# Performance work log

Measured on AMD Instinct MI355X. Metric: run time of the kernel, lower is better.

Reference implementation:

```python
import jax, jax.numpy as jnp
import numpy as np

EMBED_DIM = 2048
NUM_HEADS = 16
NUM_KV_GROUPS = 4
HEAD_DIM = EMBED_DIM // NUM_HEADS  # 128


def setup_inputs() -> dict:
    key = jax.random.key(0)
    ks = jax.random.split(key, 9)
    B, S, E = 2, 2048, EMBED_DIM
    kv_dim = HEAD_DIM * NUM_KV_GROUPS
    sc = 1.0 / np.sqrt(E)
    return {
        "x": jax.random.normal(ks[0], (B, S, E), dtype=jnp.float32),
        "Wq": jax.random.normal(ks[1], (E, E), dtype=jnp.float32) * sc,
        "bq": jnp.zeros((E,), dtype=jnp.float32),
        "Wk": jax.random.normal(ks[2], (E, kv_dim), dtype=jnp.float32) * sc,
        "bk": jnp.zeros((kv_dim,), dtype=jnp.float32),
        "Wv": jax.random.normal(ks[3], (E, kv_dim), dtype=jnp.float32) * sc,
        "bv": jnp.zeros((kv_dim,), dtype=jnp.float32),
        "Wo": jax.random.normal(ks[4], (E, E), dtype=jnp.float32) * sc,
        "bo": jnp.zeros((E,), dtype=jnp.float32),
    }


def reference(x, Wq, bq, Wk, bk, Wv, bv, Wo, bo):
    B, S, E = x.shape
    H, G, D = NUM_HEADS, NUM_KV_GROUPS, HEAD_DIM
    R = H // G  # heads per kv group
    # projections
    Q = (x @ Wq + bq).reshape(B, S, H, D).transpose(0, 2, 1, 3)   # [B,H,S,D]
    K = (x @ Wk + bk).reshape(B, S, G, D).transpose(0, 2, 1, 3)   # [B,G,S,D]
    V = (x @ Wv + bv).reshape(B, S, G, D).transpose(0, 2, 1, 3)   # [B,G,S,D]
    # GQA: broadcast KV groups over head subgroups instead of repeat_interleave copy
    Qg = Q.reshape(B, G, R, S, D)
    scores = jnp.einsum('bgrsd,bgtd->bgrst', Qg, K) / np.sqrt(D)  # [B,G,R,S,S]
    weights = jax.nn.softmax(scores, axis=-1)
    out = jnp.einsum('bgrst,bgtd->bgrsd', weights, V)             # [B,G,R,S,D]
    out = out.reshape(B, H, S, D).transpose(0, 2, 1, 3).reshape(B, S, E)
    return out @ Wo + bo
```

## Files before the change

kernel.cpp:

```cpp
#include <hip/hip_runtime.h>
#include <hip/hip_bf16.h>


typedef __attribute__((ext_vector_type(8))) short bf16x8;
typedef __attribute__((ext_vector_type(4))) short bf16x4;
typedef __attribute__((ext_vector_type(4))) float f32x4;

#define MFMA_16x16x32(a, b, c) __builtin_amdgcn_mfma_f32_16x16x32_bf16((a), (b), (c), 0, 0, 0)

__device__ __forceinline__ unsigned short f2bf(float x) {
  union { float f; unsigned int u; } c;
  c.f = x;
  unsigned int u = c.u;
  return (unsigned short)((u + 0x7fffu + ((u >> 16) & 1u)) >> 16);
}

__device__ __forceinline__ unsigned short f2bf_hw(float x) {
  __hip_bfloat16 h = __float2bfloat16(x);
  union { __hip_bfloat16 h; unsigned short u; } c;
  c.h = h;
  return c.u;
}

__device__ __forceinline__ void gload_lds16(const void* g, void* l) {
  __builtin_amdgcn_global_load_lds(
      (const __attribute__((address_space(1))) unsigned int*)g,
      (__attribute__((address_space(3))) unsigned int*)l, 16, 0, 0);
}

__global__ void cast_x_kernel(const float* __restrict__ x,
                              unsigned short* __restrict__ out, long n) {
  long i = ((long)blockIdx.x * blockDim.x + threadIdx.x) * 8;
  if (i >= n) return;
  float4 a = *reinterpret_cast<const float4*>(x + i);
  float4 b = *reinterpret_cast<const float4*>(x + i + 4);
  union { unsigned short s[8]; bf16x8 v; } o;
  o.s[0] = f2bf(a.x); o.s[1] = f2bf(a.y); o.s[2] = f2bf(a.z); o.s[3] = f2bf(a.w);
  o.s[4] = f2bf(b.x); o.s[5] = f2bf(b.y); o.s[6] = f2bf(b.z); o.s[7] = f2bf(b.w);
  *reinterpret_cast<bf16x8*>(out + i) = o.v;
}

__global__ void prep_w_kernel(const float* __restrict__ Wq,
                              const float* __restrict__ Wk,
                              const float* __restrict__ Wv,
                              const float* __restrict__ Wo,
                              unsigned short* __restrict__ WqkvT,
                              unsigned short* __restrict__ WoT) {
  __shared__ float t[32][33];
  const int tx = threadIdx.x, ty = threadIdx.y;
  const int ng = blockIdx.x * 32;
  const int k0 = blockIdx.y * 32;
  const float* src;
  int srcN, n0;
  unsigned short* dst;
  if (ng < 2048)      { src = Wq; srcN = 2048; n0 = ng;        dst = WqkvT + (size_t)ng * 2048; }
  else if (ng < 2560) { src = Wk; srcN = 512;  n0 = ng - 2048; dst = WqkvT + (size_t)ng * 2048; }
  else if (ng < 3072) { src = Wv; srcN = 512;  n0 = ng - 2560; dst = WqkvT + (size_t)ng * 2048; }
  else                { src = Wo; srcN = 2048; n0 = ng - 3072; dst = WoT + (size_t)(ng - 3072) * 2048; }
#pragma unroll
  for (int i = 0; i < 4; i++)
    t[ty + i * 8][tx] = src[(size_t)(k0 + ty + i * 8) * srcN + n0 + tx];
  __syncthreads();
#pragma unroll
  for (int i = 0; i < 4; i++)
    dst[(size_t)(ty + i * 8) * 2048 + k0 + tx] = f2bf(t[tx][ty + i * 8]);
}

__global__ void concat_bias_kernel(const float* __restrict__ bq,
                                   const float* __restrict__ bk,
                                   const float* __restrict__ bv,
                                   float* __restrict__ out) {
  int i = blockIdx.x * 256 + threadIdx.x;
  if (i >= 3072) return;
  out[i] = (i < 2048) ? bq[i] : (i < 2560 ? bk[i - 2048] : bv[i - 2560]);
}

__global__ void transpose_v_kernel(const unsigned short* __restrict__ QKV,
                                   unsigned short* __restrict__ Vt) {
  __shared__ unsigned short t[32][33];
  const int tx = threadIdx.x, ty = threadIdx.y;
  const int c0 = blockIdx.x * 32;
  const int r0 = blockIdx.y * 32;
#pragma unroll
  for (int i = 0; i < 4; i++)
    t[ty + i * 8][tx] = QKV[(size_t)(r0 + ty + i * 8) * 3072 + 2560 + c0 + tx];
  __syncthreads();
#pragma unroll
  for (int i = 0; i < 4; i++) {
    const int gd = c0 + ty + i * 8;
    const int r = r0 + tx;
    const int b = r >> 11, s = r & 2047;
    const int sp = (s & ~63) | ((s & 12) << 1) | (((s >> 4) & 1) << 2) | (s & 3) | (s & 32);
    Vt[(size_t)(b * 512 + gd) * 2048 + sp] = t[tx][ty + i * 8];
  }
}

template <int AROWS, int BROWS, bool BF16OUT>
__global__ __launch_bounds__(512, 2)
void gemm_pipe_kernel(const unsigned short* __restrict__ A,
                      const unsigned short* __restrict__ Bt,
                      const float* __restrict__ bias,
                      void* __restrict__ C, int M, int N, int K,
                      float qscale, int qcols) {
  constexpr int FM = AROWS / 32;
  constexpr int FN = BROWS / 64;
  constexpr int HFM = FM / 2;
  constexpr int TC = (AROWS + BROWS) * 4;
  constexpr int LOADS = (TC + 511) / 512;
  constexpr int PC = LOADS * 512;
  constexpr int BUFE = PC * 8;
  constexpr int BOFF = AROWS * 32;
  constexpr int LH = (LOADS + 1) / 2;
  __shared__ unsigned short lds[4 * BUFE];

  const int tid = threadIdx.x;
  const int w = tid >> 6, l = tid & 63, lg = l >> 4, ll = l & 15;
  const int wm = w >> 2, wn = w & 3;
  const int m0 = blockIdx.y * AROWS;
  const int n0 = blockIdx.x * BROWS;
  const int NT = K >> 5;

  const f32x4 fz = {0.f, 0.f, 0.f, 0.f};
  f32x4 acc[FM][FN];
#pragma unroll
  for (int i = 0; i < FM; i++)
#pragma unroll
    for (int j = 0; j < FN; j++) acc[i][j] = fz;

  const unsigned short* gsrc[LOADS];
#pragma unroll
  for (int i = 0; i < LOADS; ++i) {
    const int c = tid + 512 * i;
    if (c < AROWS * 4) {
      gsrc[i] = A + (size_t)(m0 + (c >> 2)) * K + (c & 3) * 8;
    } else if (c < TC) {
      const int cb = c - AROWS * 4;
      gsrc[i] = Bt + (size_t)(n0 + (cb >> 2)) * K + (cb & 3) * 8;
    } else {
      gsrc[i] = Bt + (size_t)n0 * K;
    }
  }

  auto stage_lo = [&](int t) {
    unsigned short* dst = &lds[(t & 3) * BUFE + tid * 8];
#pragma unroll
    for (int i = 0; i < LH; ++i) gload_lds16(gsrc[i] + t * 32, dst + i * 4096);
  };
  auto stage_hi = [&](int t) {
    unsigned short* dst = &lds[(t & 3) * BUFE + tid * 8];
#pragma unroll
    for (int i = LH; i < LOADS; ++i) gload_lds16(gsrc[i] + t * 32, dst + i * 4096);
  };

  stage_lo(0); stage_hi(0);
  stage_lo(1); stage_hi(1);

  for (int t = 0; t < NT; ++t) {
    if (t + 1 < NT) {
      if constexpr (LOADS == 4)
        asm volatile("s_waitcnt vmcnt(4)" ::: "memory");
      else if constexpr (LOADS == 3)
        asm volatile("s_waitcnt vmcnt(3)" ::: "memory");
      else
        asm volatile("s_waitcnt vmcnt(0)" ::: "memory");
    } else {
      asm volatile("s_waitcnt vmcnt(0)" ::: "memory");
    }
    __builtin_amdgcn_s_barrier();
    const unsigned short* bufp = &lds[(t & 3) * BUFE];

    bf16x8 bfrag[FN], afrag[HFM];
#pragma unroll
    for (int ni = 0; ni < FN; ++ni)
      bfrag[ni] = *reinterpret_cast<const bf16x8*>(
          &bufp[BOFF + (wn * FN * 16 + ni * 16 + ll) * 32 + lg * 8]);
#pragma unroll
    for (int mi = 0; mi < HFM; ++mi)
      afrag[mi] = *reinterpret_cast<const bf16x8*>(
          &bufp[(wm * (AROWS / 2) + mi * 16 + ll) * 32 + lg * 8]);
    if (t + 2 < NT) stage_lo(t + 2);
    __builtin_amdgcn_s_setprio(1);
#pragma unroll
    for (int mi = 0; mi < HFM; ++mi)
#pragma unroll
      for (int ni = 0; ni < FN; ++ni)
        acc[mi][ni] = MFMA_16x16x32(afrag[mi], bfrag[ni], acc[mi][ni]);
    __builtin_amdgcn_s_setprio(0);

#pragma unroll
    for (int mi = 0; mi < HFM; ++mi)
      afrag[mi] = *reinterpret_cast<const bf16x8*>(
          &bufp[(wm * (AROWS / 2) + (HFM + mi) * 16 + ll) * 32 + lg * 8]);
    if (t + 2 < NT) stage_hi(t + 2);
    __builtin_amdgcn_s_setprio(1);
#pragma unroll
    for (int mi = 0; mi < HFM; ++mi)
#pragma unroll
      for (int ni = 0; ni < FN; ++ni)
        acc[HFM + mi][ni] = MFMA_16x16x32(afrag[mi], bfrag[ni], acc[HFM + mi][ni]);
    __builtin_amdgcn_s_setprio(0);
  }

#pragma unroll
  for (int mi = 0; mi < FM; ++mi) {
#pragma unroll
    for (int ni = 0; ni < FN; ++ni) {
      const int gc = n0 + wn * FN * 16 + ni * 16 + ll;
      const float bv = bias[gc];
      const float sc = (gc < qcols) ? qscale : 1.0f;
#pragma unroll
      for (int r = 0; r < 4; ++r) {
        const int gr = m0 + wm * (AROWS / 2) + mi * 16 + 4 * lg + r;
        const float v = (acc[mi][ni][r] + bv) * sc;
        if constexpr (BF16OUT)
          ((unsigned short*)C)[(size_t)gr * N + gc] = f2bf(v);
        else
          ((float*)C)[(size_t)gr * N + gc] = v;
      }
    }
  }
}

__global__ __launch_bounds__(256, 2)
void attn_kernel(const unsigned short* __restrict__ QKV,
                 const unsigned short* __restrict__ Vt,
                 unsigned short* __restrict__ AO) {
  __shared__ unsigned short Klds[2][64 * 128];
  __shared__ unsigned short Vlds[2][128 * 64];

  const int tid = threadIdx.x;
  const int w = tid >> 6, l = tid & 63, lg = l >> 4, ll = l & 15;
  const int bh = blockIdx.y;
  const int b = bh >> 4, h = bh & 15, g = h >> 2;
  const int q0 = blockIdx.x * 128 + w * 32;
  const size_t row_base = (size_t)b * 2048 * 3072;
  const unsigned short* Vg = Vt + (size_t)(b * 512 + g * 128) * 2048;

  bf16x8 qf[2][4];
#pragma unroll
  for (int mi = 0; mi < 2; mi++)
#pragma unroll
    for (int ds = 0; ds < 4; ds++)
      qf[mi][ds] = *reinterpret_cast<const bf16x8*>(
          QKV + row_base + (size_t)(q0 + mi * 16 + ll) * 3072 + h * 128 + ds * 32 + 8 * lg);

  const f32x4 fz = {0.f, 0.f, 0.f, 0.f};
  f32x4 o[8][2];
#pragma unroll
  for (int di = 0; di < 8; di++)
#pragma unroll
    for (int mi = 0; mi < 2; mi++) o[di][mi] = fz;
  float m2[2] = {-3.0e38f, -3.0e38f}, lsum[2] = {0.f, 0.f};

  const int krow = tid >> 4, kc8 = tid & 15;
  const int vrow = tid >> 3, vc8 = tid & 7;
  const unsigned short* Kg = QKV + row_base + 2048 + g * 128 + kc8 * 8 + (size_t)krow * 3072;
  int klo[4], vlo[4];
#pragma unroll
  for (int i = 0; i < 4; i++) {
    const int kr = krow + 16 * i;
    klo[i] = (kr * 128 + kc8 * 8) ^ ((kr & 7) << 3);
    const int vr = vrow + 32 * i;
    vlo[i] = (vr * 64 + vc8 * 8) ^ ((vr & 7) << 3);
  }

  bf16x8 kreg[4], vreg[4];
#pragma unroll
  for (int i = 0; i < 4; i++) {
    kreg[i] = *reinterpret_cast<const bf16x8*>(Kg + (size_t)(16 * i) * 3072);
    vreg[i] = *reinterpret_cast<const bf16x8*>(Vg + (size_t)(vrow + 32 * i) * 2048 + vc8 * 8);
  }

  const float THR = 8.0f;

  for (int kt = 0; kt < 32; kt++) {
    const int cb = kt & 1;
#pragma unroll
    for (int i = 0; i < 4; i++) *reinterpret_cast<bf16x8*>(&Klds[cb][klo[i]]) = kreg[i];
#pragma unroll
    for (int i = 0; i < 4; i++) *reinterpret_cast<bf16x8*>(&Vlds[cb][vlo[i]]) = vreg[i];
    __syncthreads();

    if (kt + 1 < 32) {
#pragma unroll
      for (int i = 0; i < 4; i++) {
        kreg[i] = *reinterpret_cast<const bf16x8*>(
            Kg + (size_t)((kt + 1) * 64 + 16 * i) * 3072);
        vreg[i] = *reinterpret_cast<const bf16x8*>(
            Vg + (size_t)(vrow + 32 * i) * 2048 + (kt + 1) * 64 + vc8 * 8);
      }
    }

    f32x4 st[4][2];
#pragma unroll
    for (int ni = 0; ni < 4; ni++)
#pragma unroll
      for (int mi = 0; mi < 2; mi++) st[ni][mi] = fz;
#pragma unroll
    for (int ds = 0; ds < 4; ds++) {
      bf16x8 kf[4];
#pragma unroll
      for (int ni = 0; ni < 4; ni++) {
        const int kr = ni * 16 + ll;
        kf[ni] = *reinterpret_cast<const bf16x8*>(
            &Klds[cb][(kr * 128 + ds * 32 + 8 * lg) ^ ((kr & 7) << 3)]);
      }
#pragma unroll
      for (int ni = 0; ni < 4; ni++)
#pragma unroll
        for (int mi = 0; mi < 2; mi++)
          st[ni][mi] = MFMA_16x16x32(kf[ni], qf[mi][ds], st[ni][mi]);
    }

    float pm[2];
#pragma unroll
    for (int mi = 0; mi < 2; mi++) {
      float a0 = fmaxf(fmaxf(st[0][mi][0], st[0][mi][1]), st[0][mi][2]);
      float a1 = fmaxf(fmaxf(st[0][mi][3], st[1][mi][0]), st[1][mi][1]);
      float a2 = fmaxf(fmaxf(st[1][mi][2], st[1][mi][3]), st[2][mi][0]);
      float a3 = fmaxf(fmaxf(st[2][mi][1], st[2][mi][2]), st[2][mi][3]);
      float a4 = fmaxf(fmaxf(st[3][mi][0], st[3][mi][1]), st[3][mi][2]);
      pm[mi] = fmaxf(fmaxf(fmaxf(a0, a1), fmaxf(a2, a3)), fmaxf(a4, st[3][mi][3]));
      pm[mi] = fmaxf(pm[mi], __shfl_xor(pm[mi], 16, 64));
      pm[mi] = fmaxf(pm[mi], __shfl_xor(pm[mi], 32, 64));
    }
    const bool grow = (pm[0] > m2[0] + THR) || (pm[1] > m2[1] + THR);
    if (__any(grow)) {
#pragma unroll
      for (int mi = 0; mi < 2; mi++) {
        const float mn = fmaxf(m2[mi], pm[mi]);
        const float fac = __builtin_amdgcn_exp2f(m2[mi] - mn);
        m2[mi] = mn;
        lsum[mi] *= fac;
#pragma unroll
        for (int di = 0; di < 8; di++) o[di][mi] *= fac;
      }
    }
    float ps[2] = {0.f, 0.f};
#pragma unroll
    for (int ni = 0; ni < 4; ni++)
#pragma unroll
      for (int mi = 0; mi < 2; mi++)
#pragma unroll
        for (int r = 0; r < 4; r++) {
          const float pv = __builtin_amdgcn_exp2f(st[ni][mi][r] - m2[mi]);
          st[ni][mi][r] = pv;
          ps[mi] += pv;
        }
#pragma unroll
    for (int mi = 0; mi < 2; mi++) {
      ps[mi] += __shfl_xor(ps[mi], 16, 64);
      ps[mi] += __shfl_xor(ps[mi], 32, 64);
      lsum[mi] += ps[mi];
    }

    bf16x8 pf[2][2];
#pragma unroll
    for (int mi = 0; mi < 2; mi++)
#pragma unroll
      for (int ks = 0; ks < 2; ks++)
#pragma unroll
        for (int j = 0; j < 4; j++) {
          pf[mi][ks][j]     = (short)f2bf_hw(st[2 * ks][mi][j]);
          pf[mi][ks][4 + j] = (short)f2bf_hw(st[2 * ks + 1][mi][j]);
        }

#pragma unroll
    for (int ks = 0; ks < 2; ks++)
#pragma unroll
      for (int di = 0; di < 8; di++) {
        const int dr = di * 16 + ll;
        const bf16x8 vf = *reinterpret_cast<const bf16x8*>(
            &Vlds[cb][(dr * 64 + ks * 32 + 8 * lg) ^ ((dr & 7) << 3)]);
#pragma unroll
        for (int mi = 0; mi < 2; mi++)
          o[di][mi] = MFMA_16x16x32(vf, pf[mi][ks], o[di][mi]);
      }
  }

  float invl[2];
#pragma unroll
  for (int mi = 0; mi < 2; mi++) invl[mi] = 1.0f / lsum[mi];
#pragma unroll
  for (int mi = 0; mi < 2; mi++) {
    const size_t rowoff = (size_t)(b * 2048 + q0 + mi * 16 + ll) * 2048 + h * 128;
#pragma unroll
    for (int di = 0; di < 8; di++) {
      union { unsigned short s[4]; bf16x4 v; } ov;
#pragma unroll
      for (int r = 0; r < 4; r++) ov.s[r] = f2bf_hw(o[di][mi][r] * invl[mi]);
      *reinterpret_cast<bf16x4*>(&AO[rowoff + di * 16 + 4 * lg]) = ov.v;
    }
  }
}

extern "C" void kernel_launch(void* const* d_in, const int* in_sizes, int n_in,
                              void* d_out, int out_size, void* d_ws, size_t ws_size,
                              hipStream_t stream) {
  const float* x  = (const float*)d_in[0];
  const float* Wq = (const float*)d_in[1];
  const float* bq = (const float*)d_in[2];
  const float* Wk = (const float*)d_in[3];
  const float* bk = (const float*)d_in[4];
  const float* Wv = (const float*)d_in[5];
  const float* bv = (const float*)d_in[6];
  const float* Wo = (const float*)d_in[7];
  const float* bo = (const float*)d_in[8];
  float* out = (float*)d_out;

  unsigned short* xb    = (unsigned short*)d_ws;
  unsigned short* Vt    = xb;
  unsigned short* WqkvT = xb + (size_t)4096 * 2048;
  unsigned short* WoT   = WqkvT + (size_t)3072 * 2048;
  unsigned short* QKV   = WoT + (size_t)2048 * 2048;
  unsigned short* AO    = QKV + (size_t)4096 * 3072;
  float* bqkv = (float*)(AO + (size_t)4096 * 2048);

  const float QSC2 = 0.08838834764831845f * 1.4426950408889634f;

  cast_x_kernel<<<4096, 256, 0, stream>>>(x, xb, (long)8388608);
  prep_w_kernel<<<dim3(160, 64), dim3(32, 8), 0, stream>>>(Wq, Wk, Wv, Wo, WqkvT, WoT);
  concat_bias_kernel<<<12, 256, 0, stream>>>(bq, bk, bv, bqkv);

  gemm_pipe_kernel<256, 192, true><<<dim3(16, 16), 512, 0, stream>>>(
      xb, WqkvT, bqkv, QKV, 4096, 3072, 2048, QSC2, 2048);
  transpose_v_kernel<<<dim3(16, 128), dim3(32, 8), 0, stream>>>(QKV, Vt);
  attn_kernel<<<dim3(16, 32), 256, 0, stream>>>(QKV, Vt, AO);
  gemm_pipe_kernel<128, 256, false><<<dim3(8, 32), 512, 0, stream>>>(
      AO, WoT, bo, out, 4096, 2048, 2048, 1.0f, 0);
}
```

Measured before the change: 197.9 us.

## Split attention KV tiles across two wave halves and merge softmax partials in LDS

The attention kernel now launches 512 threads per block, and each query wave pair splits every 64-key tile into two 32-key halves. Each wave keeps its own running max, sum and output accumulator, and the two partial results are combined through shared memory at the end using a log-sum-exp merge. The goal is more waves in flight per CU and shorter per-wave dependency chains, so that MFMA and exp latency are better hidden. In exchange, each wave loads the full V fragment for only half the MFMA work, the final merge adds extra LDS traffic and synchronisation, and the 512,4 launch bound tightens register limits, which may cause spills of the large o accumulator.

```diff
diff --git a/kernel.cpp b/kernel.cpp
--- a/kernel.cpp
+++ b/kernel.cpp
@@ -221,18 +221,20 @@
   }
 }
 
-__global__ __launch_bounds__(256, 2)
+__global__ __launch_bounds__(512, 4)
 void attn_kernel(const unsigned short* __restrict__ QKV,
                  const unsigned short* __restrict__ Vt,
                  unsigned short* __restrict__ AO) {
-  __shared__ unsigned short Klds[2][64 * 128];
-  __shared__ unsigned short Vlds[2][128 * 64];
+  __shared__ float smem[17664];
+  unsigned short* Klds = (unsigned short*)smem;
+  unsigned short* Vlds = Klds + 2 * 64 * 128;
 
   const int tid = threadIdx.x;
   const int w = tid >> 6, l = tid & 63, lg = l >> 4, ll = l & 15;
+  const int wq = w >> 1, wk = w & 1;
   const int bh = blockIdx.y;
   const int b = bh >> 4, h = bh & 15, g = h >> 2;
-  const int q0 = blockIdx.x * 128 + w * 32;
+  const int q0 = blockIdx.x * 128 + wq * 32;
   const size_t row_base = (size_t)b * 2048 * 3072;
   const unsigned short* Vg = Vt + (size_t)(b * 512 + g * 128) * 2048;
 
@@ -252,61 +254,61 @@
     for (int mi = 0; mi < 2; mi++) o[di][mi] = fz;
   float m2[2] = {-3.0e38f, -3.0e38f}, lsum[2] = {0.f, 0.f};
 
-  const int krow = tid >> 4, kc8 = tid & 15;
-  const int vrow = tid >> 3, vc8 = tid & 7;
-  const unsigned short* Kg = QKV + row_base + 2048 + g * 128 + kc8 * 8 + (size_t)krow * 3072;
-  int klo[4], vlo[4];
-#pragma unroll
-  for (int i = 0; i < 4; i++) {
-    const int kr = krow + 16 * i;
-    klo[i] = (kr * 128 + kc8 * 8) ^ ((kr & 7) << 3);
-    const int vr = vrow + 32 * i;
-    vlo[i] = (vr * 64 + vc8 * 8) ^ ((vr & 7) << 3);
-  }
-
-  bf16x8 kreg[4], vreg[4];
-#pragma unroll
-  for (int i = 0; i < 4; i++) {
-    kreg[i] = *reinterpret_cast<const bf16x8*>(Kg + (size_t)(16 * i) * 3072);
-    vreg[i] = *reinterpret_cast<const bf16x8*>(Vg + (size_t)(vrow + 32 * i) * 2048 + vc8 * 8);
+  const int krow = tid >> 4, kcol = (tid & 15) * 8;
+  const int vrow = tid >> 3, vcol = (tid & 7) * 8;
+  const unsigned short* Kg = QKV + row_base + 2048 + g * 128 + kcol;
+  int klo[2], vlo[2];
+#pragma unroll
+  for (int i = 0; i < 2; i++) {
+    const int kr = krow + 32 * i;
+    klo[i] = (kr * 128 + kcol) ^ ((kr & 7) << 3);
+    const int vr = vrow + 64 * i;
+    vlo[i] = (vr * 64 + vcol) ^ ((vr & 7) << 3);
+  }
+
+  bf16x8 kreg[2], vreg[2];
+#pragma unroll
+  for (int i = 0; i < 2; i++) {
+    kreg[i] = *reinterpret_cast<const bf16x8*>(Kg + (size_t)(krow + 32 * i) * 3072);
+    vreg[i] = *reinterpret_cast<const bf16x8*>(Vg + (size_t)(vrow + 64 * i) * 2048 + vcol);
   }
 
   const float THR = 8.0f;
 
   for (int kt = 0; kt < 32; kt++) {
-    const int cb = kt & 1;
-#pragma unroll
-    for (int i = 0; i < 4; i++) *reinterpret_cast<bf16x8*>(&Klds[cb][klo[i]]) = kreg[i];
-#pragma unroll
-    for (int i = 0; i < 4; i++) *reinterpret_cast<bf16x8*>(&Vlds[cb][vlo[i]]) = vreg[i];
+    const int cbo = (kt & 1) * 8192;
+#pragma unroll
+    for (int i = 0; i < 2; i++) *reinterpret_cast<bf16x8*>(&Klds[cbo + klo[i]]) = kreg[i];
+#pragma unroll
+    for (int i = 0; i < 2; i++) *reinterpret_cast<bf16x8*>(&Vlds[cbo + vlo[i]]) = vreg[i];
     __syncthreads();
 
     if (kt + 1 < 32) {
 #pragma unroll
-      for (int i = 0; i < 4; i++) {
+      for (int i = 0; i < 2; i++) {
         kreg[i] = *reinterpret_cast<const bf16x8*>(
-            Kg + (size_t)((kt + 1) * 64 + 16 * i) * 3072);
+            Kg + (size_t)((kt + 1) * 64 + krow + 32 * i) * 3072);
         vreg[i] = *reinterpret_cast<const bf16x8*>(
-            Vg + (size_t)(vrow + 32 * i) * 2048 + (kt + 1) * 64 + vc8 * 8);
-      }
-    }
-
-    f32x4 st[4][2];
-#pragma unroll
-    for (int ni = 0; ni < 4; ni++)
+            Vg + (size_t)(vrow + 64 * i) * 2048 + (kt + 1) * 64 + vcol);
+      }
+    }
+
+    f32x4 st[2][2];
+#pragma unroll
+    for (int ni = 0; ni < 2; ni++)
 #pragma unroll
       for (int mi = 0; mi < 2; mi++) st[ni][mi] = fz;
 #pragma unroll
     for (int ds = 0; ds < 4; ds++) {
-      bf16x8 kf[4];
-#pragma unroll
-      for (int ni = 0; ni < 4; ni++) {
-        const int kr = ni * 16 + ll;
+      bf16x8 kf[2];
+#pragma unroll
+      for (int ni = 0; ni < 2; ni++) {
+        const int kr = wk * 32 + ni * 16 + ll;
         kf[ni] = *reinterpret_cast<const bf16x8*>(
-            &Klds[cb][(kr * 128 + ds * 32 + 8 * lg) ^ ((kr & 7) << 3)]);
-      }
-#pragma unroll
-      for (int ni = 0; ni < 4; ni++)
+            &Klds[cbo + ((kr * 128 + ds * 32 + 8 * lg) ^ ((kr & 7) << 3))]);
+      }
+#pragma unroll
+      for (int ni = 0; ni < 2; ni++)
 #pragma unroll
         for (int mi = 0; mi < 2; mi++)
           st[ni][mi] = MFMA_16x16x32(kf[ni], qf[mi][ds], st[ni][mi]);
@@ -315,12 +317,9 @@
     float pm[2];
 #pragma unroll
     for (int mi = 0; mi < 2; mi++) {
-      float a0 = fmaxf(fmaxf(st[0][mi][0], st[0][mi][1]), st[0][mi][2]);
-      float a1 = fmaxf(fmaxf(st[0][mi][3], st[1][mi][0]), st[1][mi][1]);
-      float a2 = fmaxf(fmaxf(st[1][mi][2], st[1][mi][3]), st[2][mi][0]);
-      float a3 = fmaxf(fmaxf(st[2][mi][1], st[2][mi][2]), st[2][mi][3]);
-      float a4 = fmaxf(fmaxf(st[3][mi][0], st[3][mi][1]), st[3][mi][2]);
-      pm[mi] = fmaxf(fmaxf(fmaxf(a0, a1), fmaxf(a2, a3)), fmaxf(a4, st[3][mi][3]));
+      float a0 = fmaxf(fmaxf(st[0][mi][0], st[0][mi][1]), fmaxf(st[0][mi][2], st[0][mi][3]));
+      float a1 = fmaxf(fmaxf(st[1][mi][0], st[1][mi][1]), fmaxf(st[1][mi][2], st[1][mi][3]));
+      pm[mi] = fmaxf(a0, a1);
       pm[mi] = fmaxf(pm[mi], __shfl_xor(pm[mi], 16, 64));
       pm[mi] = fmaxf(pm[mi], __shfl_xor(pm[mi], 32, 64));
     }
@@ -338,7 +337,7 @@
     }
     float ps[2] = {0.f, 0.f};
 #pragma unroll
-    for (int ni = 0; ni < 4; ni++)
+    for (int ni = 0; ni < 2; ni++)
 #pragma unroll
       for (int mi = 0; mi < 2; mi++)
 #pragma unroll
@@ -354,42 +353,65 @@
       lsum[mi] += ps[mi];
     }
 
-    bf16x8 pf[2][2];
+    bf16x8 pf[2];
 #pragma unroll
     for (int mi = 0; mi < 2; mi++)
 #pragma unroll
-      for (int ks = 0; ks < 2; ks++)
-#pragma unroll
-        for (int j = 0; j < 4; j++) {
-          pf[mi][ks][j]     = (short)f2bf_hw(st[2 * ks][mi][j]);
-          pf[mi][ks][4 + j] = (short)f2bf_hw(st[2 * ks + 1][mi][j]);
-        }
-
-#pragma unroll
-    for (int ks = 0; ks < 2; ks++)
+      for (int j = 0; j < 4; j++) {
+        pf[mi][j]     = (short)f2bf_hw(st[0][mi][j]);
+        pf[mi][4 + j] = (short)f2bf_hw(st[1][mi][j]);
+      }
+
+#pragma unroll
+    for (int di = 0; di < 8; di++) {
+      const int dr = di * 16 + ll;
+      const bf16x8 vf = *reinterpret_cast<const bf16x8*>(
+          &Vlds[cbo + ((dr * 64 + wk * 32 + 8 * lg) ^ ((dr & 7) << 3))]);
+#pragma unroll
+      for (int mi = 0; mi < 2; mi++)
+        o[di][mi] = MFMA_16x16x32(vf, pf[mi], o[di][mi]);
+    }
+  }
+
+  __syncthreads();
+  const int lb = (wq * 64 + l) * 69;
+  if (wk) {
+#pragma unroll
+    for (int di = 0; di < 8; di++)
+#pragma unroll
+      for (int mi = 0; mi < 2; mi++)
+        *reinterpret_cast<f32x4*>(&smem[lb + (di * 2 + mi) * 4]) = o[di][mi];
+    smem[lb + 64] = m2[0];
+    smem[lb + 65] = m2[1];
+    smem[lb + 66] = lsum[0];
+    smem[lb + 67] = lsum[1];
+  }
+  __syncthreads();
+  if (!wk) {
+    float al[2], bl[2];
+#pragma unroll
+    for (int mi = 0; mi < 2; mi++) {
+      const float m1 = smem[lb + 64 + mi];
+      const float l1 = smem[lb + 66 + mi];
+      const float mm = fmaxf(m2[mi], m1);
+      const float a = __builtin_amdgcn_exp2f(m2[mi] - mm);
+      const float bb = __builtin_amdgcn_exp2f(m1 - mm);
+      const float linv = 1.0f / (lsum[mi] * a + l1 * bb);
+      al[mi] = a * linv;
+      bl[mi] = bb * linv;
+    }
+#pragma unroll
+    for (int mi = 0; mi < 2; mi++) {
+      const size_t rowoff = (size_t)(b * 2048 + q0 + mi * 16 + ll) * 2048 + h * 128;
 #pragma unroll
       for (int di = 0; di < 8; di++) {
-        const int dr = di * 16 + ll;
-        const bf16x8 vf = *reinterpret_cast<const bf16x8*>(
-            &Vlds[cb][(dr * 64 + ks * 32 + 8 * lg) ^ ((dr & 7) << 3)]);
-#pragma unroll
-        for (int mi = 0; mi < 2; mi++)
-          o[di][mi] = MFMA_16x16x32(vf, pf[mi][ks], o[di][mi]);
-      }
-  }
-
-  float invl[2];
-#pragma unroll
-  for (int mi = 0; mi < 2; mi++) invl[mi] = 1.0f / lsum[mi];
-#pragma unroll
-  for (int mi = 0; mi < 2; mi++) {
-    const size_t rowoff = (size_t)(b * 2048 + q0 + mi * 16 + ll) * 2048 + h * 128;
-#pragma unroll
-    for (int di = 0; di < 8; di++) {
-      union { unsigned short s[4]; bf16x4 v; } ov;
-#pragma unroll
-      for (int r = 0; r < 4; r++) ov.s[r] = f2bf_hw(o[di][mi][r] * invl[mi]);
-      *reinterpret_cast<bf16x4*>(&AO[rowoff + di * 16 + 4 * lg]) = ov.v;
+        const f32x4 o1 = *reinterpret_cast<const f32x4*>(&smem[lb + (di * 2 + mi) * 4]);
+        union { unsigned short s[4]; bf16x4 v; } ov;
+#pragma unroll
+        for (int r = 0; r < 4; r++)
+          ov.s[r] = f2bf_hw(o[di][mi][r] * al[mi] + o1[r] * bl[mi]);
+        *reinterpret_cast<bf16x4*>(&AO[rowoff + di * 16 + 4 * lg]) = ov.v;
+      }
     }
   }
 }
@@ -425,7 +447,7 @@
   gemm_pipe_kernel<256, 192, true><<<dim3(16, 16), 512, 0, stream>>>(
       xb, WqkvT, bqkv, QKV, 4096, 3072, 2048, QSC2, 2048);
   transpose_v_kernel<<<dim3(16, 128), dim3(32, 8), 0, stream>>>(QKV, Vt);
-  attn_kernel<<<dim3(16, 32), 256, 0, stream>>>(QKV, Vt, AO);
+  attn_kernel<<<dim3(16, 32), 512, 0, stream>>>(QKV, Vt, AO);
   gemm_pipe_kernel<128, 256, false><<<dim3(8, 32), 512, 0, stream>>>(
       AO, WoT, bo, out, 4096, 2048, 2048, 1.0f, 0);
 }
```

Result: slower. 411.7 us (+108.0%).

## Stage K via direct global-to-LDS loads, read V fragments straight into registers

Applied to the files above, without the earlier changes.

The attention loop drops the register-staged K/V shared-memory double buffer. K tiles are now copied global-to-LDS asynchronously with a pre-swizzled layout, and V^T fragments are loaded directly from global memory into registers for the PV MFMAs. s_setprio hints wrap the MFMA blocks and the max reduction is rebalanced. This halves LDS use and removes VGPR staging plus LDS writes for V. The cost is a full vmcnt(0) wait each iteration and V global latency sitting on the critical path.

```diff
diff --git a/kernel.cpp b/kernel.cpp
--- a/kernel.cpp
+++ b/kernel.cpp
@@ -225,8 +225,7 @@
 void attn_kernel(const unsigned short* __restrict__ QKV,
                  const unsigned short* __restrict__ Vt,
                  unsigned short* __restrict__ AO) {
-  __shared__ unsigned short Klds[2][64 * 128];
-  __shared__ unsigned short Vlds[2][128 * 64];
+  __shared__ unsigned short Kl[2][8192];
 
   const int tid = threadIdx.x;
   const int w = tid >> 6, l = tid & 63, lg = l >> 4, ll = l & 15;
@@ -235,6 +234,21 @@
   const int q0 = blockIdx.x * 128 + w * 32;
   const size_t row_base = (size_t)b * 2048 * 3072;
   const unsigned short* Vg = Vt + (size_t)(b * 512 + g * 128) * 2048;
+  const unsigned short* Kgb = QKV + row_base + 2048 + g * 128;
+
+  int kgoff[4];
+#pragma unroll
+  for (int i = 0; i < 4; i++) {
+    const int c = i * 256 + tid;
+    const int kr = c >> 4;
+    kgoff[i] = kr * 3072 + (((c & 15) ^ (kr & 7)) << 3);
+  }
+  auto stageK = [&](int t) {
+    unsigned short* dst = &Kl[t & 1][tid * 8];
+#pragma unroll
+    for (int i = 0; i < 4; i++)
+      gload_lds16(Kgb + (size_t)t * 64 * 3072 + kgoff[i], dst + i * 2048);
+  };
 
   bf16x8 qf[2][4];
 #pragma unroll
@@ -252,44 +266,25 @@
     for (int mi = 0; mi < 2; mi++) o[di][mi] = fz;
   float m2[2] = {-3.0e38f, -3.0e38f}, lsum[2] = {0.f, 0.f};
 
-  const int krow = tid >> 4, kc8 = tid & 15;
-  const int vrow = tid >> 3, vc8 = tid & 7;
-  const unsigned short* Kg = QKV + row_base + 2048 + g * 128 + kc8 * 8 + (size_t)krow * 3072;
-  int klo[4], vlo[4];
-#pragma unroll
-  for (int i = 0; i < 4; i++) {
-    const int kr = krow + 16 * i;
-    klo[i] = (kr * 128 + kc8 * 8) ^ ((kr & 7) << 3);
-    const int vr = vrow + 32 * i;
-    vlo[i] = (vr * 64 + vc8 * 8) ^ ((vr & 7) << 3);
-  }
-
-  bf16x8 kreg[4], vreg[4];
-#pragma unroll
-  for (int i = 0; i < 4; i++) {
-    kreg[i] = *reinterpret_cast<const bf16x8*>(Kg + (size_t)(16 * i) * 3072);
-    vreg[i] = *reinterpret_cast<const bf16x8*>(Vg + (size_t)(vrow + 32 * i) * 2048 + vc8 * 8);
-  }
-
   const float THR = 8.0f;
 
+  stageK(0);
+
   for (int kt = 0; kt < 32; kt++) {
-    const int cb = kt & 1;
-#pragma unroll
-    for (int i = 0; i < 4; i++) *reinterpret_cast<bf16x8*>(&Klds[cb][klo[i]]) = kreg[i];
-#pragma unroll
-    for (int i = 0; i < 4; i++) *reinterpret_cast<bf16x8*>(&Vlds[cb][vlo[i]]) = vreg[i];
-    __syncthreads();
-
-    if (kt + 1 < 32) {
-#pragma unroll
-      for (int i = 0; i < 4; i++) {
-        kreg[i] = *reinterpret_cast<const bf16x8*>(
-            Kg + (size_t)((kt + 1) * 64 + 16 * i) * 3072);
-        vreg[i] = *reinterpret_cast<const bf16x8*>(
-            Vg + (size_t)(vrow + 32 * i) * 2048 + (kt + 1) * 64 + vc8 * 8);
-      }
-    }
+    asm volatile("s_waitcnt vmcnt(0)" ::: "memory");
+    __builtin_amdgcn_s_barrier();
+    const int kb = kt & 1;
+
+    bf16x8 vf[2][8];
+    const int vco = kt * 64 + 8 * lg;
+#pragma unroll
+    for (int ks = 0; ks < 2; ks++)
+#pragma unroll
+      for (int di = 0; di < 8; di++)
+        vf[ks][di] = *reinterpret_cast<const bf16x8*>(
+            Vg + (size_t)(di * 16 + ll) * 2048 + vco + ks * 32);
+
+    if (kt + 1 < 32) stageK(kt + 1);
 
     f32x4 st[4][2];
 #pragma unroll
@@ -303,24 +298,25 @@
       for (int ni = 0; ni < 4; ni++) {
         const int kr = ni * 16 + ll;
         kf[ni] = *reinterpret_cast<const bf16x8*>(
-            &Klds[cb][(kr * 128 + ds * 32 + 8 * lg) ^ ((kr & 7) << 3)]);
+            &Kl[kb][(kr * 128 + ds * 32 + 8 * lg) ^ ((kr & 7) << 3)]);
       }
+      __builtin_amdgcn_s_setprio(1);
 #pragma unroll
       for (int ni = 0; ni < 4; ni++)
 #pragma unroll
         for (int mi = 0; mi < 2; mi++)
           st[ni][mi] = MFMA_16x16x32(kf[ni], qf[mi][ds], st[ni][mi]);
+      __builtin_amdgcn_s_setprio(0);
     }
 
     float pm[2];
 #pragma unroll
     for (int mi = 0; mi < 2; mi++) {
-      float a0 = fmaxf(fmaxf(st[0][mi][0], st[0][mi][1]), st[0][mi][2]);
-      float a1 = fmaxf(fmaxf(st[0][mi][3], st[1][mi][0]), st[1][mi][1]);
-      float a2 = fmaxf(fmaxf(st[1][mi][2], st[1][mi][3]), st[2][mi][0]);
-      float a3 = fmaxf(fmaxf(st[2][mi][1], st[2][mi][2]), st[2][mi][3]);
-      float a4 = fmaxf(fmaxf(st[3][mi][0], st[3][mi][1]), st[3][mi][2]);
-      pm[mi] = fmaxf(fmaxf(fmaxf(a0, a1), fmaxf(a2, a3)), fmaxf(a4, st[3][mi][3]));
+      float a0 = fmaxf(fmaxf(st[0][mi][0], st[0][mi][1]), fmaxf(st[0][mi][2], st[0][mi][3]));
+      float a1 = fmaxf(fmaxf(st[1][mi][0], st[1][mi][1]), fmaxf(st[1][mi][2], st[1][mi][3]));
+      float a2 = fmaxf(fmaxf(st[2][mi][0], st[2][mi][1]), fmaxf(st[2][mi][2], st[2][mi][3]));
+      float a3 = fmaxf(fmaxf(st[3][mi][0], st[3][mi][1]), fmaxf(st[3][mi][2], st[3][mi][3]));
+      pm[mi] = fmaxf(fmaxf(a0, a1), fmaxf(a2, a3));
       pm[mi] = fmaxf(pm[mi], __shfl_xor(pm[mi], 16, 64));
       pm[mi] = fmaxf(pm[mi], __shfl_xor(pm[mi], 32, 64));
     }
@@ -365,17 +361,15 @@
           pf[mi][ks][4 + j] = (short)f2bf_hw(st[2 * ks + 1][mi][j]);
         }
 
+    __builtin_amdgcn_s_setprio(1);
 #pragma unroll
     for (int ks = 0; ks < 2; ks++)
 #pragma unroll
       for (int di = 0; di < 8; di++) {
-        const int dr = di * 16 + ll;
-        const bf16x8 vf = *reinterpret_cast<const bf16x8*>(
-            &Vlds[cb][(dr * 64 + ks * 32 + 8 * lg) ^ ((dr & 7) << 3)]);
-#pragma unroll
-        for (int mi = 0; mi < 2; mi++)
-          o[di][mi] = MFMA_16x16x32(vf, pf[mi][ks], o[di][mi]);
+        o[di][0] = MFMA_16x16x32(vf[ks][di], pf[0][ks], o[di][0]);
+        o[di][1] = MFMA_16x16x32(vf[ks][di], pf[1][ks], o[di][1]);
       }
+    __builtin_amdgcn_s_setprio(0);
   }
 
   float invl[2];
```

New measurement: 249.6 us. +26.1%, slower.
